# Performance work log

Hardware: AMD Instinct MI355X
Metric: run time of the kernel (lower is better)

Reference implementation:

```python
import jax, jax.numpy as jnp
import numpy as np

NUM_NODES = 100000
NUM_HYPEREDGES = 20000
NUM_SEMALINKS = 5000
NUM_EDGES = 600000
IN_DIM = 128
SIGNAL_DIM = 64
OUT_DIM = 128


def setup_inputs() -> dict:
    key = jax.random.key(0)
    k = jax.random.split(key, 8)
    node_embeddings = jax.random.normal(k[0], (NUM_NODES, IN_DIM), dtype=jnp.float32)
    semalink_embeddings = jax.random.normal(k[1], (NUM_SEMALINKS, SIGNAL_DIM), dtype=jnp.float32)
    hyperedge_embeddings = jax.random.normal(k[2], (NUM_HYPEREDGES, IN_DIM), dtype=jnp.float32)
    node_idx = jax.random.randint(k[3], (NUM_EDGES,), 0, NUM_NODES, dtype=jnp.int32)
    sl_idx = jax.random.randint(k[4], (NUM_EDGES,), 0, NUM_SEMALINKS, dtype=jnp.int32)
    he_idx = jax.random.randint(k[5], (NUM_EDGES,), 0, NUM_HYPEREDGES, dtype=jnp.int32)
    semalinks = jnp.stack([node_idx, sl_idx, he_idx], axis=1)  # [E, 3]
    W_a = jax.random.normal(k[6], (IN_DIM, SIGNAL_DIM), dtype=jnp.float32)
    W_f = jax.random.normal(k[7], (2 * IN_DIM, OUT_DIM), dtype=jnp.float32)
    return {
        'node_embeddings': node_embeddings,
        'semalink_embeddings': semalink_embeddings,
        'hyperedge_embeddings': hyperedge_embeddings,
        'semalinks': semalinks,
        'W_a': W_a,
        'W_f': W_f,
    }


def reference(node_embeddings, semalink_embeddings, hyperedge_embeddings, semalinks, W_a, W_f):
    # Original loops edges in order, ASSIGNING final_embeddings[node_idx] each time:
    # only the LAST edge touching each node determines that node's output.
    E = semalinks.shape[0]
    n_idx = semalinks[:, 0]
    s_idx = semalinks[:, 1]
    h_idx = semalinks[:, 2]

    order = jnp.arange(E, dtype=jnp.int32)
    last = jax.ops.segment_max(order, n_idx, num_segments=NUM_NODES)  # [N]
    has_edge = last >= 0
    last_c = jnp.clip(last, 0, E - 1)

    sel_h = h_idx[last_c]  # [N]
    sel_s = s_idx[last_c]  # [N]
    h_emb = hyperedge_embeddings[sel_h]          # [N, in_dim]
    sl_emb = semalink_embeddings[sel_s]          # [N, signal_dim]

    # per-node attention score (1x1 in original)
    r_h = node_embeddings @ W_a                  # [N, signal_dim]
    r_t = h_emb @ W_a                            # [N, signal_dim]
    score = jnp.sum(r_h * jnp.tanh(r_t + sl_emb), axis=-1, keepdims=True)  # [N, 1]
    gamma = jax.nn.softmax(score, axis=-1)       # softmax over singleton == 1.0 (same as torch)
    f = gamma * h_emb                            # [N, in_dim]

    u = jnp.concatenate([f, node_embeddings], axis=-1) @ W_f  # [N, out_dim]
    out = jnp.where(has_edge[:, None], u, jnp.zeros((), dtype=u.dtype))
    return out
```

## Files before the change

kernel.cpp:

```cpp
#include <hip/hip_runtime.h>
#include <hip/hip_bf16.h>

#define NNODES 100000
#define NHE 20000
#define NEDGES 600000

typedef float f32x4 __attribute__((ext_vector_type(4)));
typedef short bf16x8 __attribute__((ext_vector_type(8)));
typedef short bf16x4 __attribute__((ext_vector_type(4)));
typedef unsigned long long u64;

__device__ __forceinline__ unsigned short f2bf(float f) {
    unsigned u = __builtin_bit_cast(unsigned, f);
    u += 0x7fffu + ((u >> 16) & 1u);
    return (unsigned short)(u >> 16);
}
__device__ __forceinline__ float bf2f(unsigned short h) {
    unsigned u = ((unsigned)h) << 16;
    return __builtin_bit_cast(float, u);
}

__global__ void k0(u64* __restrict__ packed, const float* __restrict__ Wf,
                   unsigned short* __restrict__ wt) {
    int b = blockIdx.x, t = threadIdx.x;
    if (b < 196) {
        int i = b * 256 + t;
        if (i < NNODES / 2) ((f32x4*)packed)[i] = (f32x4){0.f, 0.f, 0.f, 0.f};
    } else {
        int idx = (b - 196) * 256 + t;
        int k = idx >> 7, c = idx & 127;
        wt[c * 256 + k] = f2bf(Wf[idx]);
    }
}

__global__ __launch_bounds__(256) void k1(
    const int* __restrict__ sl, u64* __restrict__ packed,
    const float* __restrict__ he_emb, const unsigned short* __restrict__ wt,
    unsigned short* __restrict__ heo)
{
    int b = blockIdx.x, t = threadIdx.x;
    if (b < 2344) {
        int e = b * 256 + t;
        if (e < NEDGES) {
            int n = sl[3 * e];
            int h = sl[3 * e + 2];
            atomicMax(&packed[n], ((u64)(e + 1) << 32) | (unsigned)h);
        }
        return;
    }

    __shared__ __align__(16) unsigned short Xs[64 * 128];
    int r0 = (b - 2344) * 64;

    #pragma unroll
    for (int i = 0; i < 8; ++i) {
        int idx = i * 256 + t;
        int row = idx >> 5, q = idx & 31;
        int ri = r0 + row; if (ri >= NHE) ri = NHE - 1;
        f32x4 v = *(const f32x4*)(he_emb + (long)ri * 128 + q * 4);
        bf16x4 p;
        p[0] = (short)f2bf(v[0]); p[1] = (short)f2bf(v[1]);
        p[2] = (short)f2bf(v[2]); p[3] = (short)f2bf(v[3]);
        int byte = (row * 256 + q * 8) ^ ((row & 7) << 4);
        *(bf16x4*)((char*)Xs + byte) = p;
    }
    __syncthreads();

    int lane = t & 63, w = t >> 6;
    int wm = w >> 1, wn = w & 1;
    int l15 = lane & 15, l4 = lane >> 4;

    f32x4 acc[2][4] = {};
    #pragma unroll
    for (int kc = 0; kc < 2; ++kc)
        #pragma unroll
        for (int ks = 0; ks < 2; ++ks) {
            bf16x8 a[2], bb[4];
            #pragma unroll
            for (int fm = 0; fm < 2; ++fm) {
                int row = wm * 32 + fm * 16 + l15;
                int byte = (row * 256 + kc * 128 + ks * 64 + l4 * 16) ^ ((row & 7) << 4);
                a[fm] = *(const bf16x8*)((const char*)Xs + byte);
            }
            #pragma unroll
            for (int fn = 0; fn < 4; ++fn) {
                int col = wn * 64 + fn * 16 + l15;
                bb[fn] = *(const bf16x8*)(wt + (long)col * 256 + kc * 64 + ks * 32 + l4 * 8);
            }
            #pragma unroll
            for (int fm = 0; fm < 2; ++fm)
                #pragma unroll
                for (int fn = 0; fn < 4; ++fn)
                    acc[fm][fn] = __builtin_amdgcn_mfma_f32_16x16x32_bf16(
                        a[fm], bb[fn], acc[fm][fn], 0, 0, 0);
        }

    #pragma unroll
    for (int fm = 0; fm < 2; ++fm)
        #pragma unroll
        for (int j = 0; j < 4; ++j) {
            int ri = r0 + wm * 32 + fm * 16 + l4 * 4 + j;
            if (ri < NHE) {
                #pragma unroll
                for (int fn = 0; fn < 4; ++fn) {
                    int col = wn * 64 + fn * 16 + l15;
                    heo[(long)ri * 128 + col] = f2bf(acc[fm][fn][j]);
                }
            }
        }
}

__global__ __launch_bounds__(256) void k_main(
    const float* __restrict__ node_emb,
    const u64* __restrict__ packed,
    const unsigned short* __restrict__ wt,
    const unsigned short* __restrict__ heo,
    float* __restrict__ out)
{
    __shared__ __align__(16) unsigned short Xs[64 * 128];
    __shared__ __align__(16) unsigned short Hs[64 * 128];
    __shared__ int valid_s[64];

    int t = threadIdx.x;
    int r0 = blockIdx.x * 64;
    int lane = t & 63, w = t >> 6;
    int l15 = lane & 15, l4 = lane >> 4;

    u64 p = 0;
    {
        int ri = r0 + w * 16 + l15;
        if (lane < 16 && ri < NNODES) p = packed[ri];
    }

    f32x4 nv[8];
    #pragma unroll
    for (int i = 0; i < 8; ++i) {
        int idx = i * 256 + t;
        int row = idx >> 5, q = idx & 31;
        int ri = r0 + row; if (ri >= NNODES) ri = NNODES - 1;
        nv[i] = *(const f32x4*)(node_emb + (long)ri * 128 + q * 4);
    }

    int he16 = (int)(p & 0xffffffffull);
    int v16 = (p != 0) ? 1 : 0;
    if (lane < 16) valid_s[w * 16 + l15] = v16;
    #pragma unroll
    for (int g = 0; g < 4; ++g) {
        int hrow = __shfl(he16, g * 4 + l4, 64);
        const char* gsrc = (const char*)(heo + (long)hrow * 128) + l15 * 16;
        __builtin_amdgcn_global_load_lds(
            (const __attribute__((address_space(1))) void*)gsrc,
            (__attribute__((address_space(3))) void*)&Hs[(w * 16 + g * 4) * 128],
            16, 0, 0);
    }

    #pragma unroll
    for (int i = 0; i < 8; ++i) {
        int idx = i * 256 + t;
        int row = idx >> 5, q = idx & 31;
        bf16x4 pk;
        pk[0] = (short)f2bf(nv[i][0]); pk[1] = (short)f2bf(nv[i][1]);
        pk[2] = (short)f2bf(nv[i][2]); pk[3] = (short)f2bf(nv[i][3]);
        int byte = (row * 256 + q * 8) ^ ((row & 7) << 4);
        *(bf16x4*)((char*)Xs + byte) = pk;
    }

    asm volatile("s_waitcnt lgkmcnt(0)" ::: "memory");
    __builtin_amdgcn_sched_barrier(0);
    __builtin_amdgcn_s_barrier();
    __builtin_amdgcn_sched_barrier(0);

    int wm = w >> 1, wn = w & 1;
    f32x4 acc[2][4] = {};
    #pragma unroll
    for (int kc = 0; kc < 2; ++kc)
        #pragma unroll
        for (int ks = 0; ks < 2; ++ks) {
            bf16x8 a[2], b[4];
            #pragma unroll
            for (int fm = 0; fm < 2; ++fm) {
                int row = wm * 32 + fm * 16 + l15;
                int byte = (row * 256 + kc * 128 + ks * 64 + l4 * 16) ^ ((row & 7) << 4);
                a[fm] = *(const bf16x8*)((const char*)Xs + byte);
            }
            #pragma unroll
            for (int fn = 0; fn < 4; ++fn) {
                int col = wn * 64 + fn * 16 + l15;
                b[fn] = *(const bf16x8*)(wt + (long)col * 256 + 128 + kc * 64 + ks * 32 + l4 * 8);
            }
            #pragma unroll
            for (int fm = 0; fm < 2; ++fm)
                #pragma unroll
                for (int fn = 0; fn < 4; ++fn)
                    acc[fm][fn] = __builtin_amdgcn_mfma_f32_16x16x32_bf16(
                        a[fm], b[fn], acc[fm][fn], 0, 0, 0);
        }

    asm volatile("s_waitcnt vmcnt(0) lgkmcnt(0)" ::: "memory");
    __builtin_amdgcn_sched_barrier(0);
    __builtin_amdgcn_s_barrier();
    __builtin_amdgcn_sched_barrier(0);

    #pragma unroll
    for (int fm = 0; fm < 2; ++fm)
        #pragma unroll
        for (int j = 0; j < 4; ++j) {
            int lrow = wm * 32 + fm * 16 + l4 * 4 + j;
            int ri = r0 + lrow;
            if (ri < NNODES) {
                int v = valid_s[lrow];
                #pragma unroll
                for (int fn = 0; fn < 4; ++fn) {
                    int col = wn * 64 + fn * 16 + l15;
                    float hv = bf2f(Hs[lrow * 128 + col]);
                    float val = v ? (acc[fm][fn][j] + hv) : 0.0f;
                    __builtin_nontemporal_store(val, &out[(long)ri * 128 + col]);
                }
            }
        }
}

extern "C" void kernel_launch(void* const* d_in, const int* in_sizes, int n_in,
                              void* d_out, int out_size, void* d_ws, size_t ws_size,
                              hipStream_t stream) {
    const float* node_emb = (const float*)d_in[0];
    const float* he_emb = (const float*)d_in[2];
    const int* sl = (const int*)d_in[3];
    const float* Wf = (const float*)d_in[5];
    float* out = (float*)d_out;

    u64* packed = (u64*)d_ws;
    unsigned short* wt = (unsigned short*)((char*)d_ws + 800000);
    unsigned short* heo = (unsigned short*)((char*)d_ws + 865536);

    k0<<<324, 256, 0, stream>>>(packed, Wf, wt);
    k1<<<2344 + 313, 256, 0, stream>>>(sl, packed, he_emb, wt, heo);
    k_main<<<(NNODES + 63) / 64, 256, 0, stream>>>(node_emb, packed, wt, heo, out);
}
```

Baseline: 68.90 us.

## Vectorize edge scatter and swap MFMA operands for vectorized row-major stores

The edge atomicMax pass now has each thread read four edges with three 16-byte loads instead of scalar strided loads, which cuts the block count from 2344 to 586. Both GEMMs swap their MFMA A/B operands so each lane holds four consecutive columns of one row. This allows 8-byte bf16 stores of heo and 16-byte nontemporal float4 stores of the output in place of scalar ones. The gathered hyperedge rows in LDS use an XOR swizzle on 16-byte chunks to limit bank conflicts on the new vector reads, which adds index arithmetic and a matching layout between the load and read sides.

Result: no change. 68.72 us (-0.3%).

```diff
diff --git a/kernel.cpp b/kernel.cpp
--- a/kernel.cpp
+++ b/kernel.cpp
@@ -8,6 +8,7 @@
 typedef float f32x4 __attribute__((ext_vector_type(4)));
 typedef short bf16x8 __attribute__((ext_vector_type(8)));
 typedef short bf16x4 __attribute__((ext_vector_type(4)));
+typedef int i32x4 __attribute__((ext_vector_type(4)));
 typedef unsigned long long u64;
 
 __device__ __forceinline__ unsigned short f2bf(float f) {
@@ -39,18 +40,22 @@
     unsigned short* __restrict__ heo)
 {
     int b = blockIdx.x, t = threadIdx.x;
-    if (b < 2344) {
-        int e = b * 256 + t;
-        if (e < NEDGES) {
-            int n = sl[3 * e];
-            int h = sl[3 * e + 2];
-            atomicMax(&packed[n], ((u64)(e + 1) << 32) | (unsigned)h);
+    if (b < 586) {
+        int tg = b * 256 + t;
+        if (tg < NEDGES / 4) {
+            const i32x4* s4 = (const i32x4*)sl;
+            i32x4 a = s4[3 * tg], bb = s4[3 * tg + 1], c = s4[3 * tg + 2];
+            int e0 = 4 * tg;
+            atomicMax(&packed[a[0]], ((u64)(e0 + 1) << 32) | (unsigned)a[2]);
+            atomicMax(&packed[a[3]], ((u64)(e0 + 2) << 32) | (unsigned)bb[1]);
+            atomicMax(&packed[bb[2]], ((u64)(e0 + 3) << 32) | (unsigned)c[0]);
+            atomicMax(&packed[c[1]], ((u64)(e0 + 4) << 32) | (unsigned)c[3]);
         }
         return;
     }
 
     __shared__ __align__(16) unsigned short Xs[64 * 128];
-    int r0 = (b - 2344) * 64;
+    int r0 = (b - 586) * 64;
 
     #pragma unroll
     for (int i = 0; i < 8; ++i) {
@@ -92,22 +97,24 @@
                 #pragma unroll
                 for (int fn = 0; fn < 4; ++fn)
                     acc[fm][fn] = __builtin_amdgcn_mfma_f32_16x16x32_bf16(
-                        a[fm], bb[fn], acc[fm][fn], 0, 0, 0);
-        }
-
-    #pragma unroll
-    for (int fm = 0; fm < 2; ++fm)
-        #pragma unroll
-        for (int j = 0; j < 4; ++j) {
-            int ri = r0 + wm * 32 + fm * 16 + l4 * 4 + j;
-            if (ri < NHE) {
-                #pragma unroll
-                for (int fn = 0; fn < 4; ++fn) {
-                    int col = wn * 64 + fn * 16 + l15;
-                    heo[(long)ri * 128 + col] = f2bf(acc[fm][fn][j]);
-                }
-            }
-        }
+                        bb[fn], a[fm], acc[fm][fn], 0, 0, 0);
+        }
+
+    #pragma unroll
+    for (int fm = 0; fm < 2; ++fm) {
+        int ri = r0 + wm * 32 + fm * 16 + l15;
+        if (ri < NHE) {
+            #pragma unroll
+            for (int fn = 0; fn < 4; ++fn) {
+                bf16x4 p;
+                p[0] = (short)f2bf(acc[fm][fn][0]);
+                p[1] = (short)f2bf(acc[fm][fn][1]);
+                p[2] = (short)f2bf(acc[fm][fn][2]);
+                p[3] = (short)f2bf(acc[fm][fn][3]);
+                *(bf16x4*)(heo + (long)ri * 128 + wn * 64 + fn * 16 + l4 * 4) = p;
+            }
+        }
+    }
 }
 
 __global__ __launch_bounds__(256) void k_main(
@@ -147,7 +154,8 @@
     #pragma unroll
     for (int g = 0; g < 4; ++g) {
         int hrow = __shfl(he16, g * 4 + l4, 64);
-        const char* gsrc = (const char*)(heo + (long)hrow * 128) + l15 * 16;
+        int rlow = (g * 4 + l4) & 15;
+        const char* gsrc = (const char*)(heo + (long)hrow * 128) + ((l15 ^ rlow) * 16);
         __builtin_amdgcn_global_load_lds(
             (const __attribute__((address_space(1))) void*)gsrc,
             (__attribute__((address_space(3))) void*)&Hs[(w * 16 + g * 4) * 128],
@@ -193,7 +201,7 @@
                 #pragma unroll
                 for (int fn = 0; fn < 4; ++fn)
                     acc[fm][fn] = __builtin_amdgcn_mfma_f32_16x16x32_bf16(
-                        a[fm], b[fn], acc[fm][fn], 0, 0, 0);
+                        b[fn], a[fm], acc[fm][fn], 0, 0, 0);
         }
 
     asm volatile("s_waitcnt vmcnt(0) lgkmcnt(0)" ::: "memory");
@@ -202,22 +210,25 @@
     __builtin_amdgcn_sched_barrier(0);
 
     #pragma unroll
-    for (int fm = 0; fm < 2; ++fm)
-        #pragma unroll
-        for (int j = 0; j < 4; ++j) {
-            int lrow = wm * 32 + fm * 16 + l4 * 4 + j;
-            int ri = r0 + lrow;
-            if (ri < NNODES) {
-                int v = valid_s[lrow];
+    for (int fm = 0; fm < 2; ++fm) {
+        int lrow = wm * 32 + fm * 16 + l15;
+        int ri = r0 + lrow;
+        int v = valid_s[lrow];
+        if (ri < NNODES) {
+            #pragma unroll
+            for (int fn = 0; fn < 4; ++fn) {
+                int chunk = wn * 8 + fn * 2 + (l4 >> 1);
+                int byte = lrow * 256 + ((chunk ^ l15) * 16) + (l4 & 1) * 8;
+                bf16x4 hv = *(const bf16x4*)((const char*)Hs + byte);
+                f32x4 o;
                 #pragma unroll
-                for (int fn = 0; fn < 4; ++fn) {
-                    int col = wn * 64 + fn * 16 + l15;
-                    float hv = bf2f(Hs[lrow * 128 + col]);
-                    float val = v ? (acc[fm][fn][j] + hv) : 0.0f;
-                    __builtin_nontemporal_store(val, &out[(long)ri * 128 + col]);
-                }
-            }
-        }
+                for (int jj = 0; jj < 4; ++jj)
+                    o[jj] = v ? (acc[fm][fn][jj] + bf2f((unsigned short)hv[jj])) : 0.0f;
+                __builtin_nontemporal_store(o,
+                    (f32x4*)(out + (long)ri * 128 + wn * 64 + fn * 16 + l4 * 4));
+            }
+        }
+    }
 }
 
 extern "C" void kernel_launch(void* const* d_in, const int* in_sizes, int n_in,
@@ -234,6 +245,6 @@
     unsigned short* heo = (unsigned short*)((char*)d_ws + 865536);
 
     k0<<<324, 256, 0, stream>>>(packed, Wf, wt);
-    k1<<<2344 + 313, 256, 0, stream>>>(sl, packed, he_emb, wt, heo);
+    k1<<<586 + 313, 256, 0, stream>>>(sl, packed, he_emb, wt, heo);
     k_main<<<(NNODES + 63) / 64, 256, 0, stream>>>(node_emb, packed, wt, heo, out);
 }
```
